# Kernel tuning notes

Hardware: AMD Instinct MI355X
Metric: run time of the kernel (lower is better)

## Reference

```python
import jax, jax.numpy as jnp
import numpy as np


def setup_inputs() -> dict:
    key = jax.random.key(0)
    k1, k2, k3 = jax.random.split(key, 3)
    N, S, D = 8, 2048, 1024
    x = jax.random.normal(k1, (N, S, D), dtype=jnp.float32)
    # kaiming_normal_ on a (1,1,D) tensor: std = sqrt(2 / fan_in) with fan_in = D
    std = np.sqrt(2.0 / D).astype(np.float32)
    w_lhs = jax.random.normal(k2, (1, 1, D), dtype=jnp.float32) * std
    w_rhs = jax.random.normal(k3, (1, 1, D), dtype=jnp.float32) * std
    return {"x": x, "w_lhs": w_lhs, "w_rhs": w_rhs}


def reference(x, w_lhs, w_rhs):
    # x: (N, S, D); w_lhs/w_rhs: (1, 1, D) broadcast elementwise scales
    lhs = x * w_lhs                       # (N, S, D)
    rhs = x * w_rhs                       # (N, S, D)
    scores = jnp.einsum('nsd,ntd->nst', lhs, rhs)  # (N, S, S), no 1/sqrt(d) scaling
    attn = jax.nn.softmax(scores, axis=2)
    return jnp.einsum('nst,ntd->nsd', attn, x)     # (N, S, D)
```

## Files before the change

kernel.cpp:

```cpp
#include <hip/hip_runtime.h>
#include <hip/hip_bf16.h>
#include <stdint.h>

typedef unsigned short u16;
typedef unsigned int u32;
typedef __attribute__((ext_vector_type(8))) short bf16x8;
typedef __attribute__((ext_vector_type(4))) float f32x4;

#define S_DIM 2048
#define D_DIM 1024
#define TM 128
#define TN 128
#define BK 64

__device__ __forceinline__ u16 f2bf(float f) {
  u32 u = __float_as_uint(f);
  u += 0x7FFFu + ((u >> 16) & 1u);
  return (u16)(u >> 16);
}

typedef const __attribute__((address_space(1))) u32* gas1p;
typedef __attribute__((address_space(3))) u32* las3p;

__device__ __forceinline__ void gload_lds16(const void* g, void* l) {
  __builtin_amdgcn_global_load_lds((gas1p)g, (las3p)l, 16, 0, 0);
}

__global__ __launch_bounds__(256) void prep_kernel(
    const float* __restrict__ x, const float* __restrict__ wl,
    const float* __restrict__ wr, u16* __restrict__ Qb, u16* __restrict__ Kb,
    u16* __restrict__ Vt, float* __restrict__ lsum, int batch0) {
  const int S = S_DIM, D = D_DIM;
  int nz = blockIdx.z;
  const float* xb = x + (size_t)(batch0 + nz) * S * D;
  u16* Qn = Qb + (size_t)nz * S * D;
  u16* Kn = Kb + (size_t)nz * S * D;
  u16* Vn = Vt + (size_t)nz * D * S;
  int t0 = blockIdx.x * 64;
  int d0 = blockIdx.y * 64;
  int tid = threadIdx.x;
  int rl = tid >> 4;
  int cl = (tid & 15) << 2;

  if (blockIdx.y == 0 && tid < 64) lsum[(size_t)nz * S + t0 + tid] = 0.0f;

  __shared__ u16 ldsT[64][68];

  float4 a = *(const float4*)(wl + d0 + cl);
  float4 b = *(const float4*)(wr + d0 + cl);
  float wv0 = a.x * b.x, wv1 = a.y * b.y, wv2 = a.z * b.z, wv3 = a.w * b.w;

#pragma unroll
  for (int p = 0; p < 4; ++p) {
    int r = p * 16 + rl;
    float4 xv = *(const float4*)(xb + (size_t)(t0 + r) * D + d0 + cl);
    u16 q0 = f2bf(xv.x), q1 = f2bf(xv.y), q2 = f2bf(xv.z), q3 = f2bf(xv.w);
    u16 k0 = f2bf(xv.x * wv0), k1 = f2bf(xv.y * wv1);
    u16 k2 = f2bf(xv.z * wv2), k3 = f2bf(xv.w * wv3);
    uint2 qpk;
    qpk.x = (u32)q0 | ((u32)q1 << 16);
    qpk.y = (u32)q2 | ((u32)q3 << 16);
    *(uint2*)(Qn + (size_t)(t0 + r) * D + d0 + cl) = qpk;
    uint2 kpk;
    kpk.x = (u32)k0 | ((u32)k1 << 16);
    kpk.y = (u32)k2 | ((u32)k3 << 16);
    *(uint2*)(Kn + (size_t)(t0 + r) * D + d0 + cl) = kpk;
    ldsT[cl + 0][r] = q0;
    ldsT[cl + 1][r] = q1;
    ldsT[cl + 2][r] = q2;
    ldsT[cl + 3][r] = q3;
  }
  __syncthreads();
#pragma unroll
  for (int p = 0; p < 4; ++p) {
    int dr = p * 16 + rl;
    u16 v0 = ldsT[dr][cl + 0], v1 = ldsT[dr][cl + 1];
    u16 v2 = ldsT[dr][cl + 2], v3 = ldsT[dr][cl + 3];
    uint2 pk;
    pk.x = (u32)v0 | ((u32)v1 << 16);
    pk.y = (u32)v2 | ((u32)v3 << 16);
    *(uint2*)(Vn + (size_t)(d0 + dr) * S + t0 + cl) = pk;
  }
}

__global__ __launch_bounds__(256, 2) void qk_exp_kernel(
    const u16* __restrict__ Qb, const u16* __restrict__ Kb,
    u16* __restrict__ P, float* __restrict__ lsum) {
  const int S = S_DIM, D = D_DIM;
  int nz = blockIdx.z;
  const u16* A = Qb + (size_t)nz * S * D;
  const u16* B = Kb + (size_t)nz * S * D;
  u16* C = P + (size_t)nz * S * S;
  float* lrow = lsum + (size_t)nz * S;

  int m0 = blockIdx.x * TM;
  int n0 = blockIdx.y * TN;
  int tid = threadIdx.x;
  int wave = tid >> 6;
  int lane = tid & 63;
  int lk = lane & 15;
  int g8 = lane >> 4;
  int wr = (wave >> 1) * 64;
  int wc = (wave & 1) * 64;

  __shared__ __align__(16) u16 As[TM * BK];
  __shared__ __align__(16) u16 Bs[TN * BK];

  int srow = (wave << 5) + (lane >> 3);
  int skel = ((lane & 7) ^ (lane >> 3)) << 3;
  const u16* gA = A + (size_t)(m0 + srow) * D + skel;
  const u16* gB = B + (size_t)(n0 + srow) * D + skel;

  int sx = (lane & 7) << 4;
  int aoff[4], boff[4];
#pragma unroll
  for (int i = 0; i < 4; ++i) {
    aoff[i] = ((wr + i * 16 + lk) * BK + g8 * 8) * 2;
    boff[i] = ((wc + i * 16 + lk) * BK + g8 * 8) * 2;
  }

  f32x4 acc[4][4] = {};

  for (int k0 = 0; k0 < D; k0 += BK) {
#pragma unroll
    for (int q = 0; q < 4; ++q) {
      gload_lds16(gA + (size_t)q * 8 * D, As + (wave * 4 + q) * 512);
      gload_lds16(gB + (size_t)q * 8 * D, Bs + (wave * 4 + q) * 512);
    }
    gA += BK;
    gB += BK;
    __syncthreads();
#pragma unroll
    for (int kk = 0; kk < 2; ++kk) {
      bf16x8 af[4], bfr[4];
#pragma unroll
      for (int i = 0; i < 4; ++i)
        af[i] = *(const bf16x8*)((const char*)As + ((aoff[i] + kk * 64) ^ sx));
#pragma unroll
      for (int i = 0; i < 4; ++i)
        bfr[i] = *(const bf16x8*)((const char*)Bs + ((boff[i] + kk * 64) ^ sx));
#pragma unroll
      for (int i = 0; i < 4; ++i)
#pragma unroll
        for (int j = 0; j < 4; ++j)
          acc[i][j] = __builtin_amdgcn_mfma_f32_16x16x32_bf16(af[i], bfr[j],
                                                              acc[i][j], 0, 0, 0);
    }
    __syncthreads();
  }

  int rr = g8 << 2;
#pragma unroll
  for (int i = 0; i < 4; ++i)
#pragma unroll
    for (int j = 0; j < 4; ++j)
#pragma unroll
      for (int r = 0; r < 4; ++r)
        acc[i][j][r] = __expf(fminf(acc[i][j][r], 30.0f));

#pragma unroll
  for (int i = 0; i < 4; ++i) {
#pragma unroll
    for (int r = 0; r < 4; ++r) {
      size_t row = (size_t)(m0 + wr + i * 16 + rr + r);
      u16* cp = C + row * S + n0 + wc + lk;
      cp[0] = f2bf(acc[i][0][r]);
      cp[16] = f2bf(acc[i][1][r]);
      cp[32] = f2bf(acc[i][2][r]);
      cp[48] = f2bf(acc[i][3][r]);
    }
  }

#pragma unroll
  for (int i = 0; i < 4; ++i) {
    f32x4 rs = acc[i][0] + acc[i][1] + acc[i][2] + acc[i][3];
#pragma unroll
    for (int d = 1; d < 16; d <<= 1) {
      rs[0] += __shfl_xor(rs[0], d);
      rs[1] += __shfl_xor(rs[1], d);
      rs[2] += __shfl_xor(rs[2], d);
      rs[3] += __shfl_xor(rs[3], d);
    }
    if (lk == 0) {
#pragma unroll
      for (int r = 0; r < 4; ++r)
        atomicAdd(&lrow[m0 + wr + i * 16 + rr + r], rs[r]);
    }
  }
}

__global__ __launch_bounds__(256, 2) void pv_kernel(
    const u16* __restrict__ P, const u16* __restrict__ Vt,
    const float* __restrict__ lsum, float* __restrict__ out) {
  const int S = S_DIM, D = D_DIM;
  int nz = blockIdx.z;
  const u16* A = P + (size_t)nz * S * S;
  const u16* B = Vt + (size_t)nz * D * S;
  const float* lrow = lsum + (size_t)nz * S;
  float* Cn = out + (size_t)nz * S * D;

  int m0 = blockIdx.x * TM;
  int n0 = blockIdx.y * TN;
  int tid = threadIdx.x;
  int wave = tid >> 6;
  int lane = tid & 63;
  int lk = lane & 15;
  int g8 = lane >> 4;
  int wr = (wave >> 1) * 64;
  int wc = (wave & 1) * 64;

  __shared__ __align__(16) u16 As[TM * BK];
  __shared__ __align__(16) u16 Bs[TN * BK];

  int srow = (wave << 5) + (lane >> 3);
  int skel = ((lane & 7) ^ (lane >> 3)) << 3;
  const u16* gA = A + (size_t)(m0 + srow) * S + skel;
  const u16* gB = B + (size_t)(n0 + srow) * S + skel;

  int sx = (lane & 7) << 4;
  int aoff[4], boff[4];
#pragma unroll
  for (int i = 0; i < 4; ++i) {
    aoff[i] = ((wr + i * 16 + lk) * BK + g8 * 8) * 2;
    boff[i] = ((wc + i * 16 + lk) * BK + g8 * 8) * 2;
  }

  f32x4 acc[4][4] = {};

  for (int k0 = 0; k0 < S; k0 += BK) {
#pragma unroll
    for (int q = 0; q < 4; ++q) {
      gload_lds16(gA + (size_t)q * 8 * S, As + (wave * 4 + q) * 512);
      gload_lds16(gB + (size_t)q * 8 * S, Bs + (wave * 4 + q) * 512);
    }
    gA += BK;
    gB += BK;
    __syncthreads();
#pragma unroll
    for (int kk = 0; kk < 2; ++kk) {
      bf16x8 af[4], bfr[4];
#pragma unroll
      for (int i = 0; i < 4; ++i)
        af[i] = *(const bf16x8*)((const char*)As + ((aoff[i] + kk * 64) ^ sx));
#pragma unroll
      for (int i = 0; i < 4; ++i)
        bfr[i] = *(const bf16x8*)((const char*)Bs + ((boff[i] + kk * 64) ^ sx));
#pragma unroll
      for (int i = 0; i < 4; ++i)
#pragma unroll
        for (int j = 0; j < 4; ++j)
          acc[i][j] = __builtin_amdgcn_mfma_f32_16x16x32_bf16(af[i], bfr[j],
                                                              acc[i][j], 0, 0, 0);
    }
    __syncthreads();
  }

  int rr = g8 << 2;
#pragma unroll
  for (int i = 0; i < 4; ++i) {
#pragma unroll
    for (int r = 0; r < 4; ++r) {
      int row = m0 + wr + i * 16 + rr + r;
      float inv = __fdividef(1.0f, lrow[row]);
      float* cp = Cn + (size_t)row * D + n0 + wc + lk;
      cp[0] = acc[i][0][r] * inv;
      cp[16] = acc[i][1][r] * inv;
      cp[32] = acc[i][2][r] * inv;
      cp[48] = acc[i][3][r] * inv;
    }
  }
}

extern "C" void kernel_launch(void* const* d_in, const int* in_sizes, int n_in,
                              void* d_out, int out_size, void* d_ws,
                              size_t ws_size, hipStream_t stream) {
  const float* x = (const float*)d_in[0];
  const float* wl = (const float*)d_in[1];
  const float* wr = (const float*)d_in[2];
  float* out = (float*)d_out;
  const int N = 8, S = S_DIM, D = D_DIM;
  const size_t szQ = (size_t)S * D;
  const size_t szP = (size_t)S * S;

  int g = 8;
  while (g > 1) {
    size_t need = (size_t)g * (3 * szQ * 2 + szP * 2 + (size_t)S * 4);
    if (need <= ws_size) break;
    g >>= 1;
  }

  for (int b0 = 0; b0 < N; b0 += g) {
    u16* Qb = (u16*)d_ws;
    u16* Kb = Qb + (size_t)g * szQ;
    u16* Vt = Kb + (size_t)g * szQ;
    u16* Pp = Vt + (size_t)g * szQ;
    float* lsum = (float*)(Pp + (size_t)g * szP);
    hipLaunchKernelGGL(prep_kernel, dim3(S / 64, D / 64, g), dim3(256), 0,
                       stream, x, wl, wr, Qb, Kb, Vt, lsum, b0);
    hipLaunchKernelGGL(qk_exp_kernel, dim3(S / TM, S / TN, g), dim3(256), 0,
                       stream, Qb, Kb, Pp, lsum);
    hipLaunchKernelGGL(pv_kernel, dim3(S / TM, D / TN, g), dim3(256), 0,
                       stream, Pp, Vt, lsum, out + (size_t)b0 * S * D);
  }
}
```

Before: 274.2 us.

## Use 256x256 double-buffered 8-wave GEMM core with interleaved LDS prefetch

Replaces the 128x128 single-buffered GEMM loop in both the QK-exp and PV kernels with a shared 256x256-tile, 512-thread core. The core double-buffers 128KB of LDS and splits each k-step into four MFMA quadrants, with global-to-LDS loads for the next tile interleaved between them. It also uses explicit barriers, waitcnts and setprio to overlap memory traffic with matrix math. The aim is more data reuse per tile and hidden load latency, at the cost of heavy LDS use, fewer blocks and more registers per thread.

```diff
diff --git a/kernel.cpp b/kernel.cpp
--- a/kernel.cpp
+++ b/kernel.cpp
@@ -9,9 +9,6 @@
 
 #define S_DIM 2048
 #define D_DIM 1024
-#define TM 128
-#define TN 128
-#define BK 64
 
 __device__ __forceinline__ u16 f2bf(float f) {
   u32 u = __float_as_uint(f);
@@ -24,6 +21,10 @@
 
 __device__ __forceinline__ void gload_lds16(const void* g, void* l) {
   __builtin_amdgcn_global_load_lds((gas1p)g, (las3p)l, 16, 0, 0);
+}
+
+__device__ __forceinline__ void mfma16(f32x4& c, bf16x8 a, bf16x8 b) {
+  c = __builtin_amdgcn_mfma_f32_16x16x32_bf16(a, b, c, 0, 0, 0);
 }
 
 __global__ __launch_bounds__(256) void prep_kernel(
@@ -83,7 +84,136 @@
   }
 }
 
-__global__ __launch_bounds__(256, 2) void qk_exp_kernel(
+__device__ __forceinline__ void gemm_main(const u16* __restrict__ A,
+                                          const u16* __restrict__ B, int m0,
+                                          int n0, int ldk, int NT, char* cl,
+                                          int tid, f32x4 (&acc)[8][4]) {
+  int lane = tid & 63, w = tid >> 6;
+  int lk = lane & 15, g8 = lane >> 4, l7 = lane & 7;
+  int wr = w >> 2, wc = w & 3;
+  int sA0 = (wr * 128 + lk) * 128;
+  int sB0 = (wc * 64 + lk) * 128 + 32768;
+  int sx0 = (g8 ^ l7) << 4;
+  int sx1 = ((4 + g8) ^ l7) << 4;
+  int r8 = lane >> 3;
+  int kel = (l7 ^ r8) << 3;
+  const u16* gAs = A + (size_t)(m0 + w * 16 + r8) * ldk + kel;
+  const u16* gBs = B + (size_t)(n0 + w * 16 + r8) * ldk + kel;
+  char* dA = cl + w * 2048;
+  char* dB = cl + 32768 + w * 2048;
+
+#define STG_A(kt_, h_, b_)                                                  \
+  {                                                                         \
+    const u16* g_ = gAs + (size_t)(kt_)*64 + (size_t)(h_)*128 * ldk;        \
+    char* d_ = dA + (b_)*65536 + (h_)*16384;                                \
+    gload_lds16(g_, d_);                                                    \
+    gload_lds16(g_ + 8 * (size_t)ldk, d_ + 1024);                           \
+  }
+#define STG_B(kt_, h_, b_)                                                  \
+  {                                                                         \
+    const u16* g_ = gBs + (size_t)(kt_)*64 + (size_t)(h_)*128 * ldk;        \
+    char* d_ = dB + (b_)*65536 + (h_)*16384;                                \
+    gload_lds16(g_, d_);                                                    \
+    gload_lds16(g_ + 8 * (size_t)ldk, d_ + 1024);                           \
+  }
+
+  STG_A(0, 0, 0);
+  STG_A(0, 1, 0);
+  STG_B(0, 0, 0);
+  STG_B(0, 1, 0);
+  STG_A(1, 0, 1);
+  asm volatile("s_waitcnt vmcnt(2)");
+  __builtin_amdgcn_s_barrier();
+
+  bf16x8 af0[4][2], af1[4][2], bfr[2][2];
+
+#pragma unroll 1
+  for (int kt = 0; kt < NT; ++kt) {
+    int b = kt & 1, nb = b ^ 1;
+    int bo = b * 65536;
+#pragma unroll
+    for (int m = 0; m < 4; ++m) {
+      af0[m][0] = *(const bf16x8*)(cl + bo + sA0 + m * 2048 + sx0);
+      af0[m][1] = *(const bf16x8*)(cl + bo + sA0 + m * 2048 + sx1);
+    }
+#pragma unroll
+    for (int n = 0; n < 2; ++n) {
+      bfr[n][0] = *(const bf16x8*)(cl + bo + sB0 + n * 2048 + sx0);
+      bfr[n][1] = *(const bf16x8*)(cl + bo + sB0 + n * 2048 + sx1);
+    }
+    if (kt + 1 < NT) STG_A(kt + 1, 1, nb);
+    __builtin_amdgcn_s_barrier();
+    asm volatile("s_waitcnt lgkmcnt(0)");
+    __builtin_amdgcn_s_setprio(1);
+#pragma unroll
+    for (int m = 0; m < 4; ++m)
+#pragma unroll
+      for (int n = 0; n < 2; ++n) {
+        mfma16(acc[m][n], af0[m][0], bfr[n][0]);
+        mfma16(acc[m][n], af0[m][1], bfr[n][1]);
+      }
+    __builtin_amdgcn_s_setprio(0);
+    __builtin_amdgcn_s_barrier();
+#pragma unroll
+    for (int m = 0; m < 4; ++m) {
+      af1[m][0] = *(const bf16x8*)(cl + bo + sA0 + (m + 4) * 2048 + sx0);
+      af1[m][1] = *(const bf16x8*)(cl + bo + sA0 + (m + 4) * 2048 + sx1);
+    }
+    if (kt + 1 < NT) STG_B(kt + 1, 0, nb);
+    __builtin_amdgcn_s_barrier();
+    asm volatile("s_waitcnt lgkmcnt(0)");
+    __builtin_amdgcn_s_setprio(1);
+#pragma unroll
+    for (int m = 0; m < 4; ++m)
+#pragma unroll
+      for (int n = 0; n < 2; ++n) {
+        mfma16(acc[m + 4][n], af1[m][0], bfr[n][0]);
+        mfma16(acc[m + 4][n], af1[m][1], bfr[n][1]);
+      }
+    __builtin_amdgcn_s_setprio(0);
+    __builtin_amdgcn_s_barrier();
+#pragma unroll
+    for (int n = 0; n < 2; ++n) {
+      bfr[n][0] = *(const bf16x8*)(cl + bo + sB0 + (n + 2) * 2048 + sx0);
+      bfr[n][1] = *(const bf16x8*)(cl + bo + sB0 + (n + 2) * 2048 + sx1);
+    }
+    if (kt + 1 < NT) STG_B(kt + 1, 1, nb);
+    __builtin_amdgcn_s_barrier();
+    asm volatile("s_waitcnt lgkmcnt(0)");
+    __builtin_amdgcn_s_setprio(1);
+#pragma unroll
+    for (int m = 0; m < 4; ++m)
+#pragma unroll
+      for (int n = 0; n < 2; ++n) {
+        mfma16(acc[m][n + 2], af0[m][0], bfr[n][0]);
+        mfma16(acc[m][n + 2], af0[m][1], bfr[n][1]);
+      }
+    __builtin_amdgcn_s_setprio(0);
+    __builtin_amdgcn_s_barrier();
+    if (kt + 2 < NT) STG_A(kt + 2, 0, b);
+    __builtin_amdgcn_s_barrier();
+    asm volatile("s_waitcnt lgkmcnt(0)");
+    __builtin_amdgcn_s_setprio(1);
+#pragma unroll
+    for (int m = 0; m < 4; ++m)
+#pragma unroll
+      for (int n = 0; n < 2; ++n) {
+        mfma16(acc[m + 4][n + 2], af1[m][0], bfr[n][0]);
+        mfma16(acc[m + 4][n + 2], af1[m][1], bfr[n][1]);
+      }
+    __builtin_amdgcn_s_setprio(0);
+    if (kt + 2 < NT) {
+      asm volatile("s_waitcnt vmcnt(2)");
+    } else {
+      asm volatile("s_waitcnt vmcnt(0)");
+    }
+    __builtin_amdgcn_s_barrier();
+  }
+#undef STG_A
+#undef STG_B
+}
+
+__global__ __launch_bounds__(512, 2) void qk_exp_kernel(
     const u16* __restrict__ Qb, const u16* __restrict__ Kb,
     u16* __restrict__ P, float* __restrict__ lsum) {
   const int S = S_DIM, D = D_DIM;
@@ -93,87 +223,31 @@
   u16* C = P + (size_t)nz * S * S;
   float* lrow = lsum + (size_t)nz * S;
 
-  int m0 = blockIdx.x * TM;
-  int n0 = blockIdx.y * TN;
+  int m0 = blockIdx.x * 256;
+  int n0 = blockIdx.y * 256;
   int tid = threadIdx.x;
-  int wave = tid >> 6;
-  int lane = tid & 63;
-  int lk = lane & 15;
-  int g8 = lane >> 4;
-  int wr = (wave >> 1) * 64;
-  int wc = (wave & 1) * 64;
-
-  __shared__ __align__(16) u16 As[TM * BK];
-  __shared__ __align__(16) u16 Bs[TN * BK];
-
-  int srow = (wave << 5) + (lane >> 3);
-  int skel = ((lane & 7) ^ (lane >> 3)) << 3;
-  const u16* gA = A + (size_t)(m0 + srow) * D + skel;
-  const u16* gB = B + (size_t)(n0 + srow) * D + skel;
-
-  int sx = (lane & 7) << 4;
-  int aoff[4], boff[4];
-#pragma unroll
-  for (int i = 0; i < 4; ++i) {
-    aoff[i] = ((wr + i * 16 + lk) * BK + g8 * 8) * 2;
-    boff[i] = ((wc + i * 16 + lk) * BK + g8 * 8) * 2;
-  }
-
-  f32x4 acc[4][4] = {};
-
-  for (int k0 = 0; k0 < D; k0 += BK) {
-#pragma unroll
-    for (int q = 0; q < 4; ++q) {
-      gload_lds16(gA + (size_t)q * 8 * D, As + (wave * 4 + q) * 512);
-      gload_lds16(gB + (size_t)q * 8 * D, Bs + (wave * 4 + q) * 512);
-    }
-    gA += BK;
-    gB += BK;
-    __syncthreads();
-#pragma unroll
-    for (int kk = 0; kk < 2; ++kk) {
-      bf16x8 af[4], bfr[4];
-#pragma unroll
-      for (int i = 0; i < 4; ++i)
-        af[i] = *(const bf16x8*)((const char*)As + ((aoff[i] + kk * 64) ^ sx));
-#pragma unroll
-      for (int i = 0; i < 4; ++i)
-        bfr[i] = *(const bf16x8*)((const char*)Bs + ((boff[i] + kk * 64) ^ sx));
-#pragma unroll
-      for (int i = 0; i < 4; ++i)
-#pragma unroll
-        for (int j = 0; j < 4; ++j)
-          acc[i][j] = __builtin_amdgcn_mfma_f32_16x16x32_bf16(af[i], bfr[j],
-                                                              acc[i][j], 0, 0, 0);
-    }
-    __syncthreads();
-  }
-
+
+  __shared__ __align__(16) u16 lds[65536];
+  f32x4 acc[8][4] = {};
+  gemm_main(A, B, m0, n0, D, D / 64, (char*)lds, tid, acc);
+
+  int lane = tid & 63, w = tid >> 6;
+  int lk = lane & 15, g8 = lane >> 4;
+  int wr = w >> 2, wc = w & 3;
   int rr = g8 << 2;
 #pragma unroll
-  for (int i = 0; i < 4; ++i)
-#pragma unroll
-    for (int j = 0; j < 4; ++j)
-#pragma unroll
-      for (int r = 0; r < 4; ++r)
-        acc[i][j][r] = __expf(fminf(acc[i][j][r], 30.0f));
-
-#pragma unroll
-  for (int i = 0; i < 4; ++i) {
-#pragma unroll
-    for (int r = 0; r < 4; ++r) {
-      size_t row = (size_t)(m0 + wr + i * 16 + rr + r);
-      u16* cp = C + row * S + n0 + wc + lk;
-      cp[0] = f2bf(acc[i][0][r]);
-      cp[16] = f2bf(acc[i][1][r]);
-      cp[32] = f2bf(acc[i][2][r]);
-      cp[48] = f2bf(acc[i][3][r]);
-    }
-  }
-
-#pragma unroll
-  for (int i = 0; i < 4; ++i) {
-    f32x4 rs = acc[i][0] + acc[i][1] + acc[i][2] + acc[i][3];
+  for (int m = 0; m < 8; ++m) {
+    int rowb = m0 + wr * 128 + m * 16 + rr;
+    float rs[4] = {0.f, 0.f, 0.f, 0.f};
+#pragma unroll
+    for (int n = 0; n < 4; ++n) {
+#pragma unroll
+      for (int r = 0; r < 4; ++r) {
+        float e = __expf(fminf(acc[m][n][r], 30.0f));
+        rs[r] += e;
+        C[(size_t)(rowb + r) * S + n0 + wc * 64 + n * 16 + lk] = f2bf(e);
+      }
+    }
 #pragma unroll
     for (int d = 1; d < 16; d <<= 1) {
       rs[0] += __shfl_xor(rs[0], d);
@@ -183,13 +257,12 @@
     }
     if (lk == 0) {
 #pragma unroll
-      for (int r = 0; r < 4; ++r)
-        atomicAdd(&lrow[m0 + wr + i * 16 + rr + r], rs[r]);
-    }
-  }
-}
-
-__global__ __launch_bounds__(256, 2) void pv_kernel(
+      for (int r = 0; r < 4; ++r) atomicAdd(&lrow[rowb + r], rs[r]);
+    }
+  }
+}
+
+__global__ __launch_bounds__(512, 2) void pv_kernel(
     const u16* __restrict__ P, const u16* __restrict__ Vt,
     const float* __restrict__ lsum, float* __restrict__ out) {
   const int S = S_DIM, D = D_DIM;
@@ -199,74 +272,29 @@
   const float* lrow = lsum + (size_t)nz * S;
   float* Cn = out + (size_t)nz * S * D;
 
-  int m0 = blockIdx.x * TM;
-  int n0 = blockIdx.y * TN;
+  int m0 = blockIdx.x * 256;
+  int n0 = blockIdx.y * 256;
   int tid = threadIdx.x;
-  int wave = tid >> 6;
-  int lane = tid & 63;
-  int lk = lane & 15;
-  int g8 = lane >> 4;
-  int wr = (wave >> 1) * 64;
-  int wc = (wave & 1) * 64;
-
-  __shared__ __align__(16) u16 As[TM * BK];
-  __shared__ __align__(16) u16 Bs[TN * BK];
-
-  int srow = (wave << 5) + (lane >> 3);
-  int skel = ((lane & 7) ^ (lane >> 3)) << 3;
-  const u16* gA = A + (size_t)(m0 + srow) * S + skel;
-  const u16* gB = B + (size_t)(n0 + srow) * S + skel;
-
-  int sx = (lane & 7) << 4;
-  int aoff[4], boff[4];
-#pragma unroll
-  for (int i = 0; i < 4; ++i) {
-    aoff[i] = ((wr + i * 16 + lk) * BK + g8 * 8) * 2;
-    boff[i] = ((wc + i * 16 + lk) * BK + g8 * 8) * 2;
-  }
-
-  f32x4 acc[4][4] = {};
-
-  for (int k0 = 0; k0 < S; k0 += BK) {
-#pragma unroll
-    for (int q = 0; q < 4; ++q) {
-      gload_lds16(gA + (size_t)q * 8 * S, As + (wave * 4 + q) * 512);
-      gload_lds16(gB + (size_t)q * 8 * S, Bs + (wave * 4 + q) * 512);
-    }
-    gA += BK;
-    gB += BK;
-    __syncthreads();
-#pragma unroll
-    for (int kk = 0; kk < 2; ++kk) {
-      bf16x8 af[4], bfr[4];
-#pragma unroll
-      for (int i = 0; i < 4; ++i)
-        af[i] = *(const bf16x8*)((const char*)As + ((aoff[i] + kk * 64) ^ sx));
-#pragma unroll
-      for (int i = 0; i < 4; ++i)
-        bfr[i] = *(const bf16x8*)((const char*)Bs + ((boff[i] + kk * 64) ^ sx));
-#pragma unroll
-      for (int i = 0; i < 4; ++i)
-#pragma unroll
-        for (int j = 0; j < 4; ++j)
-          acc[i][j] = __builtin_amdgcn_mfma_f32_16x16x32_bf16(af[i], bfr[j],
-                                                              acc[i][j], 0, 0, 0);
-    }
-    __syncthreads();
-  }
-
+
+  __shared__ __align__(16) u16 lds[65536];
+  f32x4 acc[8][4] = {};
+  gemm_main(A, B, m0, n0, S, S / 64, (char*)lds, tid, acc);
+
+  int lane = tid & 63, w = tid >> 6;
+  int lk = lane & 15, g8 = lane >> 4;
+  int wr = w >> 2, wc = w & 3;
   int rr = g8 << 2;
 #pragma unroll
-  for (int i = 0; i < 4; ++i) {
+  for (int m = 0; m < 8; ++m) {
+    int rowb = m0 + wr * 128 + m * 16 + rr;
 #pragma unroll
     for (int r = 0; r < 4; ++r) {
-      int row = m0 + wr + i * 16 + rr + r;
-      float inv = __fdividef(1.0f, lrow[row]);
-      float* cp = Cn + (size_t)row * D + n0 + wc + lk;
-      cp[0] = acc[i][0][r] * inv;
-      cp[16] = acc[i][1][r] * inv;
-      cp[32] = acc[i][2][r] * inv;
-      cp[48] = acc[i][3][r] * inv;
+      float inv = __fdividef(1.0f, lrow[rowb + r]);
+      float* cp = Cn + (size_t)(rowb + r) * D + n0 + wc * 64 + lk;
+      cp[0] = acc[m][0][r] * inv;
+      cp[16] = acc[m][1][r] * inv;
+      cp[32] = acc[m][2][r] * inv;
+      cp[48] = acc[m][3][r] * inv;
     }
   }
 }
@@ -297,9 +325,9 @@
     float* lsum = (float*)(Pp + (size_t)g * szP);
     hipLaunchKernelGGL(prep_kernel, dim3(S / 64, D / 64, g), dim3(256), 0,
                        stream, x, wl, wr, Qb, Kb, Vt, lsum, b0);
-    hipLaunchKernelGGL(qk_exp_kernel, dim3(S / TM, S / TN, g), dim3(256), 0,
+    hipLaunchKernelGGL(qk_exp_kernel, dim3(S / 256, S / 256, g), dim3(512), 0,
                        stream, Qb, Kb, Pp, lsum);
-    hipLaunchKernelGGL(pv_kernel, dim3(S / TM, D / TN, g), dim3(256), 0,
+    hipLaunchKernelGGL(pv_kernel, dim3(S / 256, D / 256, g), dim3(512), 0,
                        stream, Pp, Vt, lsum, out + (size_t)b0 * S * D);
   }
 }
```

After: 270.7 us. Within noise of the previous version (-1.3%).
